# Kernel optimization log

Measured on AMD Instinct MI355X. Metric: run time of the kernel, lower is better.

Reference implementation:

```python
import jax, jax.numpy as jnp
import numpy as np

T_MAX = 16           # max target instance label (labels 1..T_MAX, 0 = background)
CCL_ITERS = 128      # fixed label-propagation iterations for connected components
S1 = 0.7310585786300049    # sigmoid(1.0)
SP0 = 0.6931471805599453   # softplus(0.0) = log 2
SP1 = 1.3132616875182228   # softplus(1.0)


def bce_dice(logits, target):
    # BCEDiceLoss: BCE-with-logits (mean) + soft dice on sigmoid probs
    p = jax.nn.sigmoid(logits)
    bce = jnp.mean(jax.nn.softplus(logits) - logits * target)
    inter = jnp.sum(p * target)
    dice = 1.0 - (2.0 * inter + 1.0) / (jnp.sum(p) + jnp.sum(target) + 1.0)
    return bce + dice


def connected_components(mask):
    # 4-connected components via iterative max-label propagation.
    # mask: [B,H,W] bool. Returns int32 label map; component id = max flat index in component + 1.
    B, H, W = mask.shape
    init = jnp.where(mask, jnp.arange(1, B * H * W + 1, dtype=jnp.int32).reshape(B, H, W), 0)

    def step(lab, _):
        up = jnp.pad(lab, ((0, 0), (1, 0), (0, 0)))[:, :H, :]
        dn = jnp.pad(lab, ((0, 0), (0, 1), (0, 0)))[:, 1:, :]
        lf = jnp.pad(lab, ((0, 0), (0, 0), (1, 0)))[:, :, :W]
        rt = jnp.pad(lab, ((0, 0), (0, 0), (0, 1)))[:, :, 1:]
        nb = jnp.maximum(jnp.maximum(up, dn), jnp.maximum(lf, rt))
        return jnp.where(mask, jnp.maximum(lab, nb), 0), None

    lab, _ = jax.lax.scan(step, init, None, length=CCL_ITERS)
    return lab


def _forward(pred_out, target_mask):
    B, C, H, W = pred_out.shape
    N = B * H * W
    Nf = jnp.float32(N)

    pm = jnp.argmax(pred_out, axis=1)          # [B,H,W] in {0,1} since C=2
    fg = pm > 0                                 # predicted foreground

    # base loss on channel-1 logits masked to predicted foreground vs binarized target
    res = bce_dice(pred_out[:, 1:2] * fg[:, None].astype(pred_out.dtype),
                   (target_mask > 0).astype(jnp.float32))

    # relabel predicted foreground into connected components (global unique ids)
    lab = connected_components(fg)              # [B,H,W]
    comp = jnp.where(fg, lab - 1, 0).reshape(-1)          # component root id in [0,N)
    tgt = target_mask[:, 0].reshape(-1).astype(jnp.int32)  # target label 0..T_MAX
    w = fg.reshape(-1).astype(jnp.float32)

    # confusion counts: inter[p, t] = |{pixels: pred comp p AND target label t}|
    inter = jax.ops.segment_sum(w, comp * (T_MAX + 1) + tgt,
                                num_segments=N * (T_MAX + 1)).reshape(N, T_MAX + 1)
    cnt_p = inter.sum(axis=1)                                       # [N] pred comp sizes
    cnt_t = jax.ops.segment_sum(jnp.ones((N,), jnp.float32), tgt,
                                num_segments=T_MAX + 1)             # [T+1] target sizes

    def pair_losses(inter_t, ct):
        # BCEDice between binary comp mask (as logits in {0,1}) and binary target mask,
        # expressed in closed form from the confusion counts.
        bce = (Nf * SP0 + cnt_p * (SP1 - SP0) - inter_t) / Nf
        sum_pt = 0.5 * ct + (S1 - 0.5) * inter_t
        sum_p = 0.5 * Nf + (S1 - 0.5) * cnt_p
        dice = 1.0 - (2.0 * sum_pt + 1.0) / (sum_p + ct + 1.0)
        return bce + dice

    def step(carry, t):
        used, acc, matched, un_tgt = carry
        ct = cnt_t[t]
        present = ct > 0
        avail = (cnt_p > 0) & (~used)
        any_avail = jnp.any(avail)
        losses = jnp.where(avail, pair_losses(inter[:, t], ct), jnp.inf)
        idx = jnp.argmin(losses)
        do = present & any_avail
        acc = acc + jnp.where(do, losses[idx], 0.0)
        used = used.at[idx].set(used[idx] | do)
        matched = matched + do.astype(jnp.float32)
        un_tgt = un_tgt + (present & (~any_avail)).astype(jnp.float32)
        return (used, acc, matched, un_tgt), None

    carry0 = (jnp.zeros((N,), bool), res, jnp.float32(0.0), jnp.float32(0.0))
    (used, acc, matched, un_tgt), _ = jax.lax.scan(step, carry0, jnp.arange(1, T_MAX + 1))

    n_pred = jnp.sum((cnt_p > 0).astype(jnp.float32))   # total pred components
    return acc + (n_pred - matched) + un_tgt            # penalties for unmatched comps/targets


def setup_inputs() -> dict:
    key = jax.random.key(0)
    k1, k2 = jax.random.split(key)
    pred_out = jax.random.normal(k1, (4, 2, 512, 512), dtype=jnp.float32)
    target_mask = jax.random.randint(k2, (4, 1, 512, 512), 0, 17, dtype=jnp.int32)
    return {"pred_out": pred_out, "target_mask": target_mask}


def reference(pred_out, target_mask):
    return _forward(pred_out, target_mask)
```

## Files before the change

kernel.cpp:

```cpp
#include <hip/hip_runtime.h>
#include <math.h>

#define HH 512
#define WW 512
#define HWSZ (HH * WW)
#define NB 4
#define NPIX (NB * HWSZ)
#define TMAX 16

#define CAP 131072
#define NPART 24
#define NBLK 1024
#define SBLK 512
#define RSTRIDE 20

#define TS 32
#define SEAMS 15
#define EDGES_PER_DIR (NB * SEAMS * HH)
#define NEDGES (2 * EDGES_PER_DIR)
#define BORDER_BLOCKS 64

struct Scalars {
  double sums[4];
  int cnt_t[TMAX + 1];
  int n_comp;
};

__device__ __forceinline__ float pair_loss(float cp, float it, float ctf) {
  const float Nf = (float)NPIX;
  float bce = (Nf * 0.69314718f + cp * 0.62011451f - it) / Nf;
  float sum_pt = 0.5f * ctf + 0.23105858f * it;
  float sum_p = 0.5f * Nf + 0.23105858f * cp;
  float dice = 1.0f - (2.0f * sum_pt + 1.0f) / (sum_p + ctf + 1.0f);
  return bce + dice;
}

__device__ __forceinline__ int chaseRO(const int* __restrict__ P, int x) {
  int p = P[x];
  while (p != x) { x = p; p = P[x]; }
  return x;
}
__device__ __forceinline__ int findRootH(int* P, int x) {
  int p = P[x];
  while (p != x) {
    int gp = P[p];
    if (gp == p) return p;
    P[x] = gp;
    x = gp; p = P[x];
  }
  return x;
}
__device__ void unite(int* P, int a, int b) {
  a = findRootH(P, a);
  b = findRootH(P, b);
  for (;;) {
    if (a == b) return;
    if (a > b) { int t = a; a = b; b = t; }
    int old = atomicMax(&P[a], b);
    if (old == a) return;
    a = findRootH(P, old);
    b = findRootH(P, b);
  }
}
__device__ __forceinline__ int findL(const int* lp, int x) {
  int p = lp[x];
  while (p != x) { x = p; p = lp[x]; }
  return x;
}
__device__ void uniteL(int* lp, int a, int b) {
  a = findL(lp, a);
  b = findL(lp, b);
  for (;;) {
    if (a == b) return;
    if (a > b) { int t = a; a = b; b = t; }
    int old = atomicMax(&lp[a], b);
    if (old == a) return;
    a = findL(lp, old);
    b = findL(lp, b);
  }
}

__global__ __launch_bounds__(256) void k_tile(const float* __restrict__ pred,
                                              const int* __restrict__ tgt,
                                              int* __restrict__ P,
                                              double* __restrict__ part) {
  __shared__ int lp[TS * TS];
  __shared__ int hist[TMAX + 1];
  __shared__ double red[4][4];
  int tid = threadIdx.x, bid = blockIdx.x;
  if (tid <= TMAX) hist[tid] = 0;
  int b = bid >> 8;
  int ty = (bid >> 4) & 15, tx = bid & 15;
  int gbase = b * HWSZ + ((ty << 5) << 9) + (tx << 5);
  int c0 = tid << 2;
  int hw0 = (gbase - b * HWSZ) + ((c0 >> 5) << 9) + (c0 & 31);
  int gi0 = b * HWSZ + hw0;
  const float* pb = pred + ((size_t)(b << 1)) * HWSZ;
  float4 p0 = *(const float4*)(pb + hw0);
  float4 p1 = *(const float4*)(pb + HWSZ + hw0);
  int4 tv = *(const int4*)(tgt + gi0);
  __syncthreads();

  float s0 = 0.f, s1 = 0.f, s2 = 0.f, s3 = 0.f;
#define ELEM(P0, P1, TV, K)                                      \
  {                                                              \
    bool fg = (P1) > (P0);                                       \
    float logit = fg ? (P1) : 0.0f;                              \
    float tb = ((TV) > 0) ? 1.0f : 0.0f;                         \
    float sp = fmaxf(logit, 0.0f) + log1pf(expf(-fabsf(logit))); \
    s0 += sp - logit * tb;                                       \
    float pr = 1.0f / (1.0f + expf(-logit));                     \
    s1 += pr; s2 += pr * tb; s3 += tb;                           \
    atomicAdd(&hist[TV], 1);                                     \
    lp[c0 + (K)] = fg ? (c0 + (K)) : -1;                         \
  }
  ELEM(p0.x, p1.x, tv.x, 0)
  ELEM(p0.y, p1.y, tv.y, 1)
  ELEM(p0.z, p1.z, tv.z, 2)
  ELEM(p0.w, p1.w, tv.w, 3)
#undef ELEM
  __syncthreads();

#pragma unroll
  for (int k = 0; k < 4; ++k) {
    int c = (k << 8) + tid;
    if (lp[c] >= 0) {
      int r = c >> 5, q = c & 31;
      if (q < TS - 1 && lp[c + 1] >= 0)  uniteL(lp, c, c + 1);
      if (r < TS - 1 && lp[c + TS] >= 0) uniteL(lp, c, c + TS);
    }
  }
  __syncthreads();
#pragma unroll
  for (int k = 0; k < 4; ++k) {
    int c = (k << 8) + tid;
    int gi = gbase + ((c >> 5) << 9) + (c & 31);
    if (lp[c] >= 0) {
      int rr = findL(lp, c);
      P[gi] = gbase + ((rr >> 5) << 9) + (rr & 31);
    } else {
      P[gi] = -1;
    }
  }

  for (int o = 32; o > 0; o >>= 1) {
    s0 += __shfl_down(s0, o);
    s1 += __shfl_down(s1, o);
    s2 += __shfl_down(s2, o);
    s3 += __shfl_down(s3, o);
  }
  int lane = tid & 63, wid = tid >> 6;
  if (!lane) { red[wid][0] = s0; red[wid][1] = s1; red[wid][2] = s2; red[wid][3] = s3; }
  __syncthreads();
  double* row = part + (size_t)bid * NPART;
  if (tid <= TMAX) row[4 + tid] = (double)hist[tid];
  if (!tid) {
    row[0] = red[0][0] + red[1][0] + red[2][0] + red[3][0];
    row[1] = red[0][1] + red[1][1] + red[2][1] + red[3][1];
    row[2] = red[0][2] + red[1][2] + red[2][2] + red[3][2];
    row[3] = red[0][3] + red[1][3] + red[2][3] + red[3][3];
  }
}

__global__ __launch_bounds__(256) void k_border(int* __restrict__ P,
                                                const double* __restrict__ part,
                                                Scalars* __restrict__ sc) {
  int tid = threadIdx.x;
  int bid = blockIdx.x;
  if (bid == 0) {
    int lane = tid & 63, wv = tid >> 6;
    double v[21];
#pragma unroll
    for (int j = 0; j < 21; ++j) v[j] = 0.0;
    for (int r = tid; r < NBLK; r += 256) {
      const double* row = part + (size_t)r * NPART;
#pragma unroll
      for (int j = 0; j < 21; ++j) v[j] += row[j];
    }
#pragma unroll
    for (int o = 32; o > 0; o >>= 1) {
#pragma unroll
      for (int j = 0; j < 21; ++j) v[j] += __shfl_down(v[j], o);
    }
    __shared__ double redr[4][21];
    if (!lane) {
#pragma unroll
      for (int j = 0; j < 21; ++j) redr[wv][j] = v[j];
    }
    __syncthreads();
    if (!tid) {
#pragma unroll
      for (int j = 0; j < 21; ++j) v[j] = redr[0][j] + redr[1][j] + redr[2][j] + redr[3][j];
      sc->sums[0] = v[0]; sc->sums[1] = v[1]; sc->sums[2] = v[2]; sc->sums[3] = v[3];
      for (int j = 0; j <= TMAX; ++j) sc->cnt_t[j] = (int)(v[4 + j] + 0.5);
    }
  }
  for (int e = bid * 256 + tid; e < NEDGES; e += BORDER_BLOCKS * 256) {
    int dir = e >= EDGES_PER_DIR;
    int e2 = dir ? e - EDGES_PER_DIR : e;
    int b = e2 / (SEAMS * HH);
    int r2 = e2 - b * (SEAMS * HH);
    int seam = r2 >> 9;
    int pos = r2 & 511;
    int i, j;
    if (!dir) {
      int w = (TS - 1) + (seam << 5);
      i = b * HWSZ + (pos << 9) + w;
      j = i + 1;
    } else {
      int h = (TS - 1) + (seam << 5);
      i = b * HWSZ + (h << 9) + pos;
      j = i + WW;
    }
    if (P[i] >= 0 && P[j] >= 0) unite(P, i, j);
  }
}

__global__ __launch_bounds__(256) void k_flatb(int* __restrict__ P,
                                               int* __restrict__ bcnt) {
  __shared__ int redi[4];
  int tid = threadIdx.x;
  int g = blockIdx.x * 256 + tid;
  int i0 = g << 2;
  int4 pv = *(const int4*)(P + i0);
  int4 rv;
  rv.x = (pv.x < 0) ? -1 : chaseRO(P, pv.x);
  rv.y = (pv.y < 0) ? -1 : chaseRO(P, pv.y);
  rv.z = (pv.z < 0) ? -1 : chaseRO(P, pv.z);
  rv.w = (pv.w < 0) ? -1 : chaseRO(P, pv.w);
  *(int4*)(P + i0) = rv;
  int c = (rv.x == i0 + 0) + (rv.y == i0 + 1) + (rv.z == i0 + 2) + (rv.w == i0 + 3);
  for (int o = 32; o > 0; o >>= 1) c += __shfl_down(c, o);
  int lane = tid & 63, wv = tid >> 6;
  if (!lane) redi[wv] = c;
  __syncthreads();
  if (!tid) bcnt[blockIdx.x] = redi[0] + redi[1] + redi[2] + redi[3];
}

__global__ __launch_bounds__(256) void k_scatter(const int* __restrict__ P,
                                                 const int* __restrict__ bcnt,
                                                 int* __restrict__ dof,
                                                 int* __restrict__ interD,
                                                 Scalars* __restrict__ sc) {
  __shared__ int redi[4];
  __shared__ int redp4[4];
  __shared__ int wtot[4];
  int tid = threadIdx.x;
  int bid = blockIdx.x;
  int lane = tid & 63, wv = tid >> 6;
  int i0 = (bid << 10) + (tid << 2);
  int4 rv = *(const int4*)(P + i0);
  int isr[4] = { rv.x == i0 + 0, rv.y == i0 + 1, rv.z == i0 + 2, rv.w == i0 + 3 };
  int cme = isr[0] + isr[1] + isr[2] + isr[3];
  int4 bv = *(const int4*)(bcnt + (tid << 2));
  int j0 = tid << 2;
  int tot = bv.x + bv.y + bv.z + bv.w;
  int pre = ((j0 + 0 < bid) ? bv.x : 0) + ((j0 + 1 < bid) ? bv.y : 0)
          + ((j0 + 2 < bid) ? bv.z : 0) + ((j0 + 3 < bid) ? bv.w : 0);
  for (int o = 32; o > 0; o >>= 1) {
    tot += __shfl_down(tot, o);
    pre += __shfl_down(pre, o);
  }
  if (!lane) { redi[wv] = tot; redp4[wv] = pre; }
  __syncthreads();
  tot = redi[0] + redi[1] + redi[2] + redi[3];
  pre = redp4[0] + redp4[1] + redp4[2] + redp4[3];
  if (bid == 0 && tid == 0) sc->n_comp = tot;
  int v = cme;
  for (int o = 1; o < 64; o <<= 1) {
    int u = __shfl_up(v, o);
    if (lane >= o) v += u;
  }
  if (lane == 63) wtot[wv] = v;
  __syncthreads();
  int add = 0;
  for (int w = 0; w < wv; ++w) add += wtot[w];
  int d = pre + v + add - cme;
#pragma unroll
  for (int k = 0; k < 4; ++k) {
    if (isr[k]) { dof[i0 + k] = d; ++d; }
  }
  int btot = wtot[0] + wtot[1] + wtot[2] + wtot[3];
  size_t zs = (size_t)pre * RSTRIDE;
  size_t ze = (size_t)(pre + btot) * RSTRIDE;
  size_t zcap = (size_t)CAP * RSTRIDE;
  if (ze > zcap) ze = zcap;
  for (size_t j = zs + tid; j < ze; j += 256) interD[j] = 0;
}

__global__ __launch_bounds__(256) void k_interall(const int* __restrict__ P,
                                                  const int* __restrict__ tgt,
                                                  const int* __restrict__ dof,
                                                  int* __restrict__ interD) {
  int g = blockIdx.x * 256 + threadIdx.x;
  int i0 = g << 2;
  int4 rv = *(const int4*)(P + i0);
  int4 tv = *(const int4*)(tgt + i0);
#define DO(R, T)                                                     \
  if ((R) >= 0) {                                                    \
    int dd = dof[R];                                                 \
    if ((unsigned)dd < CAP) atomicAdd(&interD[(size_t)dd * RSTRIDE + (T)], 1); \
  }
  DO(rv.x, tv.x) DO(rv.y, tv.y) DO(rv.z, tv.z) DO(rv.w, tv.w)
#undef DO
}

__global__ __launch_bounds__(256) void k_scanmins(const Scalars* __restrict__ sc,
                                                  const int* __restrict__ interD,
                                                  unsigned long long* __restrict__ bm) {
  int tid = threadIdx.x;
  int d = blockIdx.x * 256 + tid;
  int n_comp = sc->n_comp;
  if (n_comp > CAP) n_comp = CAP;
  int row[RSTRIDE];
  int cp = 0;
  if (d < n_comp) {
    const int4* rp = (const int4*)(interD + (size_t)d * RSTRIDE);
#pragma unroll
    for (int k = 0; k < 5; ++k) {
      int4 r4 = rp[k];
      row[(k << 2) + 0] = r4.x; row[(k << 2) + 1] = r4.y;
      row[(k << 2) + 2] = r4.z; row[(k << 2) + 3] = r4.w;
      cp += r4.x + r4.y + r4.z + r4.w;
    }
  }
  __shared__ unsigned long long wmin[4][16];
  float cpf = (float)cp;
  int lane = tid & 63, wv = tid >> 6;
#pragma unroll
  for (int t = 1; t <= TMAX; ++t) {
    unsigned long long key = ~0ULL;
    if (d < n_comp) {
      float loss = pair_loss(cpf, (float)row[t], (float)sc->cnt_t[t]);
      key = ((unsigned long long)__float_as_uint(loss) << 32) | (unsigned)d;
    }
    for (int o = 32; o > 0; o >>= 1) {
      unsigned long long kk = __shfl_down(key, o);
      if (kk < key) key = kk;
    }
    if (!lane) wmin[wv][t - 1] = key;
  }
  __syncthreads();
  if (tid < 16) {
    unsigned long long m = wmin[0][tid];
    if (wmin[1][tid] < m) m = wmin[1][tid];
    if (wmin[2][tid] < m) m = wmin[2][tid];
    if (wmin[3][tid] < m) m = wmin[3][tid];
    bm[(size_t)tid * SBLK + blockIdx.x] = m;
  }
}

__global__ __launch_bounds__(1024) void k_greedy(const Scalars* __restrict__ sc,
                                                 const int* __restrict__ interD,
                                                 const unsigned long long* __restrict__ bm,
                                                 float* __restrict__ out) {
  __shared__ unsigned long long lbm[16 * SBLK];
  int tid = threadIdx.x;
  int lane = tid & 63;
#pragma unroll
  for (int k = 0; k < 8; ++k) lbm[tid + (k << 10)] = bm[tid + (k << 10)];
  __syncthreads();

  int n_comp = sc->n_comp;
  if (n_comp > CAP) n_comp = CAP;
  double acc = 0.0;
  int matched = 0, un = 0, nused = 0;
  int used_reg = -1;

  for (int t = 1; t <= TMAX; ++t) {
    int ct = sc->cnt_t[t];
    if (ct == 0) continue;
    const int rowoff = (t - 1) * SBLK;
    for (int iter = 0; iter < 40; ++iter) {
      unsigned long long key = lbm[rowoff + lane];
#pragma unroll
      for (int k = 1; k < 8; ++k) {
        unsigned long long kk = lbm[rowoff + lane + (k << 6)];
        if (kk < key) key = kk;
      }
      for (int o = 32; o > 0; o >>= 1) {
        unsigned long long kk = __shfl_xor(key, o);
        if (kk < key) key = kk;
      }
      if (key == ~0ULL) { un += 1; break; }
      int dd = (int)(key & 0xFFFFFFFFu);
      bool ex = false;
      for (int u = 0; u < nused; ++u) {
        int uid = __shfl(used_reg, u);
        if (uid == dd) { ex = true; break; }
      }
      if (!ex) {
        acc += (double)__uint_as_float((unsigned)(key >> 32));
        matched += 1;
        if (lane == nused) used_reg = dd;
        nused += 1;
        break;
      }
      int b = dd >> 8;
      unsigned long long nk = ~0ULL;
#pragma unroll
      for (int k = 0; k < 4; ++k) {
        int d2 = (b << 8) + lane + (k << 6);
        if (d2 < n_comp) {
          bool ex2 = false;
          for (int u = 0; u < nused; ++u) {
            int uid = __shfl(used_reg, u);
            if (uid == d2) { ex2 = true; break; }
          }
          if (!ex2) {
            const int* rrow = interD + (size_t)d2 * RSTRIDE;
            int c = 0;
#pragma unroll
            for (int j = 0; j < RSTRIDE; ++j) c += rrow[j];
            float loss = pair_loss((float)c, (float)rrow[t], (float)ct);
            unsigned long long cand = ((unsigned long long)__float_as_uint(loss) << 32) | (unsigned)d2;
            if (cand < nk) nk = cand;
          }
        }
      }
      for (int o = 32; o > 0; o >>= 1) {
        unsigned long long kk = __shfl_xor(nk, o);
        if (kk < nk) nk = kk;
      }
      __syncthreads();
      if (!tid) lbm[rowoff + b] = nk;
      __syncthreads();
    }
  }

  if (!tid) {
    double Nd = (double)NPIX;
    double res = sc->sums[0] / Nd
               + 1.0 - (2.0 * sc->sums[2] + 1.0) / (sc->sums[1] + sc->sums[3] + 1.0);
    out[0] = (float)(res + acc + (double)(n_comp - matched) + (double)un);
  }
}

extern "C" void kernel_launch(void* const* d_in, const int* in_sizes, int n_in,
                              void* d_out, int out_size, void* d_ws, size_t ws_size,
                              hipStream_t stream) {
  (void)in_sizes; (void)n_in; (void)out_size; (void)ws_size;
  const float* pred = (const float*)d_in[0];
  const int* tgt = (const int*)d_in[1];
  float* out = (float*)d_out;

  char* w = (char*)d_ws;
  int* P     = (int*)w;            w += (size_t)NPIX * 4;
  int* dof   = (int*)w;            w += (size_t)NPIX * 4;
  double* part = (double*)w;       w += (size_t)NBLK * NPART * 8;
  Scalars* sc = (Scalars*)w;       w += 256;
  int* bcnt  = (int*)w;            w += 4096;
  unsigned long long* bm = (unsigned long long*)w; w += (size_t)16 * SBLK * 8;
  int* interD = (int*)w;

  k_tile<<<NBLK, 256, 0, stream>>>(pred, tgt, P, part);
  k_border<<<BORDER_BLOCKS, 256, 0, stream>>>(P, part, sc);
  k_flatb<<<NBLK, 256, 0, stream>>>(P, bcnt);
  k_scatter<<<NBLK, 256, 0, stream>>>(P, bcnt, dof, interD, sc);
  k_interall<<<NBLK, 256, 0, stream>>>(P, tgt, dof, interD);
  k_scanmins<<<SBLK, 256, 0, stream>>>(sc, interD, bm);
  k_greedy<<<1, 1024, 0, stream>>>(sc, interD, bm, out);
}
```

Measured before the change: 124.6 us.

## Fuse flatten and scatter via decoupled block-count publishing; halve scanmins blocks

```diff
diff --git a/kernel.cpp b/kernel.cpp
--- a/kernel.cpp
+++ b/kernel.cpp
@@ -11,8 +11,10 @@
 #define CAP 131072
 #define NPART 24
 #define NBLK 1024
-#define SBLK 512
+#define SMB 256
 #define RSTRIDE 20
+#define FLAGBIT 0x80000000u
+#define POLLCAP (1 << 22)
 
 #define TS 32
 #define SEAMS 15
@@ -83,11 +85,13 @@
 __global__ __launch_bounds__(256) void k_tile(const float* __restrict__ pred,
                                               const int* __restrict__ tgt,
                                               int* __restrict__ P,
-                                              double* __restrict__ part) {
+                                              double* __restrict__ part,
+                                              unsigned* __restrict__ state) {
   __shared__ int lp[TS * TS];
   __shared__ int hist[TMAX + 1];
   __shared__ double red[4][4];
   int tid = threadIdx.x, bid = blockIdx.x;
+  if (!tid) state[bid] = 0;
   if (tid <= TMAX) hist[tid] = 0;
   int b = bid >> 8;
   int ty = (bid >> 4) & 15, tx = bid & 15;
@@ -216,12 +220,18 @@
   }
 }
 
-__global__ __launch_bounds__(256) void k_flatb(int* __restrict__ P,
-                                               int* __restrict__ bcnt) {
+__global__ __launch_bounds__(256) void k_flatscan(int* __restrict__ P,
+                                                  unsigned* __restrict__ state,
+                                                  int* __restrict__ dof,
+                                                  int* __restrict__ interD,
+                                                  Scalars* __restrict__ sc) {
   __shared__ int redi[4];
+  __shared__ int redp[4];
+  __shared__ int wtot[4];
   int tid = threadIdx.x;
-  int g = blockIdx.x * 256 + tid;
-  int i0 = g << 2;
+  int bid = blockIdx.x;
+  int lane = tid & 63, wv = tid >> 6;
+  int i0 = (bid << 10) + (tid << 2);
   int4 pv = *(const int4*)(P + i0);
   int4 rv;
   rv.x = (pv.x < 0) ? -1 : chaseRO(P, pv.x);
@@ -229,43 +239,28 @@
   rv.z = (pv.z < 0) ? -1 : chaseRO(P, pv.z);
   rv.w = (pv.w < 0) ? -1 : chaseRO(P, pv.w);
   *(int4*)(P + i0) = rv;
-  int c = (rv.x == i0 + 0) + (rv.y == i0 + 1) + (rv.z == i0 + 2) + (rv.w == i0 + 3);
-  for (int o = 32; o > 0; o >>= 1) c += __shfl_down(c, o);
-  int lane = tid & 63, wv = tid >> 6;
-  if (!lane) redi[wv] = c;
-  __syncthreads();
-  if (!tid) bcnt[blockIdx.x] = redi[0] + redi[1] + redi[2] + redi[3];
-}
-
-__global__ __launch_bounds__(256) void k_scatter(const int* __restrict__ P,
-                                                 const int* __restrict__ bcnt,
-                                                 int* __restrict__ dof,
-                                                 int* __restrict__ interD,
-                                                 Scalars* __restrict__ sc) {
-  __shared__ int redi[4];
-  __shared__ int redp4[4];
-  __shared__ int wtot[4];
-  int tid = threadIdx.x;
-  int bid = blockIdx.x;
-  int lane = tid & 63, wv = tid >> 6;
-  int i0 = (bid << 10) + (tid << 2);
-  int4 rv = *(const int4*)(P + i0);
   int isr[4] = { rv.x == i0 + 0, rv.y == i0 + 1, rv.z == i0 + 2, rv.w == i0 + 3 };
   int cme = isr[0] + isr[1] + isr[2] + isr[3];
-  int4 bv = *(const int4*)(bcnt + (tid << 2));
-  int j0 = tid << 2;
-  int tot = bv.x + bv.y + bv.z + bv.w;
-  int pre = ((j0 + 0 < bid) ? bv.x : 0) + ((j0 + 1 < bid) ? bv.y : 0)
-          + ((j0 + 2 < bid) ? bv.z : 0) + ((j0 + 3 < bid) ? bv.w : 0);
-  for (int o = 32; o > 0; o >>= 1) {
-    tot += __shfl_down(tot, o);
-    pre += __shfl_down(pre, o);
-  }
-  if (!lane) { redi[wv] = tot; redp4[wv] = pre; }
-  __syncthreads();
-  tot = redi[0] + redi[1] + redi[2] + redi[3];
-  pre = redp4[0] + redp4[1] + redp4[2] + redp4[3];
-  if (bid == 0 && tid == 0) sc->n_comp = tot;
+  int c = cme;
+  for (int o = 32; o > 0; o >>= 1) c += __shfl_down(c, o);
+  if (!lane) redi[wv] = c;
+  __syncthreads();
+  int btot = redi[0] + redi[1] + redi[2] + redi[3];
+  if (!tid) atomicExch(&state[bid], (unsigned)btot | FLAGBIT);
+
+  int pre = 0;
+  for (int j = tid; j < bid; j += 256) {
+    unsigned v;
+    int guard = 0;
+    do { v = atomicAdd(&state[j], 0u); } while (!(v & FLAGBIT) && ++guard < POLLCAP);
+    pre += (int)(v & 0x7FFFFFFFu);
+  }
+  for (int o = 32; o > 0; o >>= 1) pre += __shfl_down(pre, o);
+  if (!lane) redp[wv] = pre;
+  __syncthreads();
+  int PRE = redp[0] + redp[1] + redp[2] + redp[3];
+  if (bid == NBLK - 1 && !tid) sc->n_comp = PRE + btot;
+
   int v = cme;
   for (int o = 1; o < 64; o <<= 1) {
     int u = __shfl_up(v, o);
@@ -275,14 +270,13 @@
   __syncthreads();
   int add = 0;
   for (int w = 0; w < wv; ++w) add += wtot[w];
-  int d = pre + v + add - cme;
+  int d = PRE + v + add - cme;
 #pragma unroll
   for (int k = 0; k < 4; ++k) {
     if (isr[k]) { dof[i0 + k] = d; ++d; }
   }
-  int btot = wtot[0] + wtot[1] + wtot[2] + wtot[3];
-  size_t zs = (size_t)pre * RSTRIDE;
-  size_t ze = (size_t)(pre + btot) * RSTRIDE;
+  size_t zs = (size_t)PRE * RSTRIDE;
+  size_t ze = (size_t)(PRE + btot) * RSTRIDE;
   size_t zcap = (size_t)CAP * RSTRIDE;
   if (ze > zcap) ze = zcap;
   for (size_t j = zs + tid; j < ze; j += 256) interD[j] = 0;
@@ -309,30 +303,47 @@
                                                   const int* __restrict__ interD,
                                                   unsigned long long* __restrict__ bm) {
   int tid = threadIdx.x;
-  int d = blockIdx.x * 256 + tid;
   int n_comp = sc->n_comp;
   if (n_comp > CAP) n_comp = CAP;
-  int row[RSTRIDE];
-  int cp = 0;
-  if (d < n_comp) {
-    const int4* rp = (const int4*)(interD + (size_t)d * RSTRIDE);
+  int d0 = (blockIdx.x << 9) + tid;
+  int d1 = d0 + 256;
+  int r0[RSTRIDE], r1[RSTRIDE];
+  int cp0 = 0, cp1 = 0;
+  if (d0 < n_comp) {
+    const int4* rp = (const int4*)(interD + (size_t)d0 * RSTRIDE);
 #pragma unroll
     for (int k = 0; k < 5; ++k) {
       int4 r4 = rp[k];
-      row[(k << 2) + 0] = r4.x; row[(k << 2) + 1] = r4.y;
-      row[(k << 2) + 2] = r4.z; row[(k << 2) + 3] = r4.w;
-      cp += r4.x + r4.y + r4.z + r4.w;
+      r0[(k << 2) + 0] = r4.x; r0[(k << 2) + 1] = r4.y;
+      r0[(k << 2) + 2] = r4.z; r0[(k << 2) + 3] = r4.w;
+      cp0 += r4.x + r4.y + r4.z + r4.w;
+    }
+  }
+  if (d1 < n_comp) {
+    const int4* rp = (const int4*)(interD + (size_t)d1 * RSTRIDE);
+#pragma unroll
+    for (int k = 0; k < 5; ++k) {
+      int4 r4 = rp[k];
+      r1[(k << 2) + 0] = r4.x; r1[(k << 2) + 1] = r4.y;
+      r1[(k << 2) + 2] = r4.z; r1[(k << 2) + 3] = r4.w;
+      cp1 += r4.x + r4.y + r4.z + r4.w;
     }
   }
   __shared__ unsigned long long wmin[4][16];
-  float cpf = (float)cp;
+  float cf0 = (float)cp0, cf1 = (float)cp1;
   int lane = tid & 63, wv = tid >> 6;
 #pragma unroll
   for (int t = 1; t <= TMAX; ++t) {
     unsigned long long key = ~0ULL;
-    if (d < n_comp) {
-      float loss = pair_loss(cpf, (float)row[t], (float)sc->cnt_t[t]);
-      key = ((unsigned long long)__float_as_uint(loss) << 32) | (unsigned)d;
+    float ctf = (float)sc->cnt_t[t];
+    if (d0 < n_comp) {
+      float loss = pair_loss(cf0, (float)r0[t], ctf);
+      key = ((unsigned long long)__float_as_uint(loss) << 32) | (unsigned)d0;
+    }
+    if (d1 < n_comp) {
+      float loss = pair_loss(cf1, (float)r1[t], ctf);
+      unsigned long long k2 = ((unsigned long long)__float_as_uint(loss) << 32) | (unsigned)d1;
+      if (k2 < key) key = k2;
     }
     for (int o = 32; o > 0; o >>= 1) {
       unsigned long long kk = __shfl_down(key, o);
@@ -346,7 +357,7 @@
     if (wmin[1][tid] < m) m = wmin[1][tid];
     if (wmin[2][tid] < m) m = wmin[2][tid];
     if (wmin[3][tid] < m) m = wmin[3][tid];
-    bm[(size_t)tid * SBLK + blockIdx.x] = m;
+    bm[(size_t)tid * SMB + blockIdx.x] = m;
   }
 }
 
@@ -354,11 +365,11 @@
                                                  const int* __restrict__ interD,
                                                  const unsigned long long* __restrict__ bm,
                                                  float* __restrict__ out) {
-  __shared__ unsigned long long lbm[16 * SBLK];
+  __shared__ unsigned long long lbm[16 * SMB];
   int tid = threadIdx.x;
   int lane = tid & 63;
 #pragma unroll
-  for (int k = 0; k < 8; ++k) lbm[tid + (k << 10)] = bm[tid + (k << 10)];
+  for (int k = 0; k < 4; ++k) lbm[tid + (k << 10)] = bm[tid + (k << 10)];
   __syncthreads();
 
   int n_comp = sc->n_comp;
@@ -370,11 +381,11 @@
   for (int t = 1; t <= TMAX; ++t) {
     int ct = sc->cnt_t[t];
     if (ct == 0) continue;
-    const int rowoff = (t - 1) * SBLK;
+    const int rowoff = (t - 1) * SMB;
     for (int iter = 0; iter < 40; ++iter) {
       unsigned long long key = lbm[rowoff + lane];
 #pragma unroll
-      for (int k = 1; k < 8; ++k) {
+      for (int k = 1; k < 4; ++k) {
         unsigned long long kk = lbm[rowoff + lane + (k << 6)];
         if (kk < key) key = kk;
       }
@@ -396,11 +407,11 @@
         nused += 1;
         break;
       }
-      int b = dd >> 8;
+      int b = dd >> 9;
       unsigned long long nk = ~0ULL;
 #pragma unroll
-      for (int k = 0; k < 4; ++k) {
-        int d2 = (b << 8) + lane + (k << 6);
+      for (int k = 0; k < 8; ++k) {
+        int d2 = (b << 9) + lane + (k << 6);
         if (d2 < n_comp) {
           bool ex2 = false;
           for (int u = 0; u < nused; ++u) {
@@ -449,15 +460,14 @@
   int* dof   = (int*)w;            w += (size_t)NPIX * 4;
   double* part = (double*)w;       w += (size_t)NBLK * NPART * 8;
   Scalars* sc = (Scalars*)w;       w += 256;
-  int* bcnt  = (int*)w;            w += 4096;
-  unsigned long long* bm = (unsigned long long*)w; w += (size_t)16 * SBLK * 8;
+  unsigned* state = (unsigned*)w;  w += 4096;
+  unsigned long long* bm = (unsigned long long*)w; w += (size_t)16 * SMB * 8;
   int* interD = (int*)w;
 
-  k_tile<<<NBLK, 256, 0, stream>>>(pred, tgt, P, part);
+  k_tile<<<NBLK, 256, 0, stream>>>(pred, tgt, P, part, state);
   k_border<<<BORDER_BLOCKS, 256, 0, stream>>>(P, part, sc);
-  k_flatb<<<NBLK, 256, 0, stream>>>(P, bcnt);
-  k_scatter<<<NBLK, 256, 0, stream>>>(P, bcnt, dof, interD, sc);
+  k_flatscan<<<NBLK, 256, 0, stream>>>(P, state, dof, interD, sc);
   k_interall<<<NBLK, 256, 0, stream>>>(P, tgt, dof, interD);
-  k_scanmins<<<SBLK, 256, 0, stream>>>(sc, interD, bm);
+  k_scanmins<<<SMB, 256, 0, stream>>>(sc, interD, bm);
   k_greedy<<<1, 1024, 0, stream>>>(sc, interD, bm, out);
 }
```

Measured after the change: 131.6 us. 1.06x slower.
